# Optimization experiments

Measured on AMD Instinct MI355X. Metric: run time of the kernel, lower is better.

Reference implementation:

```python
import jax, jax.numpy as jnp
import numpy as np

B, NQ, NK, D = 16, 256, 256, 256  # batch, n_queries, n_keys, kq_size (=value_size)


def setup_inputs() -> dict:
    key = jax.random.key(0)
    ks = jax.random.split(key, 8)
    s1 = 1.0 / np.sqrt(2 * D)  # fan-in scaled init for W1 (split into Wk, Wq)
    s2 = 1.0 / np.sqrt(D)
    return {
        "keys": jax.random.normal(ks[0], (B, NK, D), jnp.float32),
        "queries": jax.random.normal(ks[1], (B, NQ, D), jnp.float32),
        "values": jax.random.normal(ks[2], (B, NK, D), jnp.float32),
        # MLP layer 1: Linear(2*D -> D); concat(keys, queries) @ W1 == keys@Wk + queries@Wq
        "Wk": jax.random.normal(ks[3], (D, D), jnp.float32) * s1,
        "Wq": jax.random.normal(ks[4], (D, D), jnp.float32) * s1,
        "b1": jax.random.normal(ks[5], (D,), jnp.float32) * 0.01,
        # MLP layer 2: Linear(D -> 1)
        "w2": jax.random.normal(ks[6], (D,), jnp.float32) * s2,
        "b2": jax.random.normal(ks[7], (1,), jnp.float32) * 0.01,
    }


def reference(keys, queries, values, Wk, Wq, b1, w2, b2):
    # Additive (Bahdanau) attention: score(q,k) = w2 . tanh(W1 @ [k; q] + b1) + b2
    hk = jnp.einsum("bkd,de->bke", keys, Wk)      # [B,K,D]
    hq = jnp.einsum("bqd,de->bqe", queries, Wq)   # [B,Q,D]
    h = jnp.tanh(hq[:, :, None, :] + hk[:, None, :, :] + b1)  # [B,Q,K,D]
    logits = jnp.einsum("bqkd,d->bqk", h, w2) + b2[0]          # [B,Q,K]
    attn = jax.nn.softmax(logits, axis=-1)                     # normalize over keys
    context = jnp.einsum("bqk,bkv->bqv", attn, values)         # [B,Q,Dv]
    return context
```

## Files before the change

### kernel.cpp

```cpp
#include <hip/hip_runtime.h>
#include <hip/hip_bf16.h>

#ifndef __has_builtin
#define __has_builtin(x) 0
#endif

__device__ __forceinline__ float fast_exp2(float x) {
#if __has_builtin(__builtin_amdgcn_exp2f)
  return __builtin_amdgcn_exp2f(x);
#else
  return __exp2f(x);
#endif
}
__device__ __forceinline__ float fast_rcp(float x) {
#if __has_builtin(__builtin_amdgcn_rcpf)
  return __builtin_amdgcn_rcpf(x);
#else
  return 1.0f / x;
#endif
}

#define B_   16
#define NQ_  256
#define NK_  256
#define D_   256
#define QT   4
#define TANH_SCALE 2.8853900817779268f
#define NEG2LOG2E  (-2.8853900817779268f)

__global__ __launch_bounds__(256) void proj_kernel(
    const float* __restrict__ queries, const float* __restrict__ keys,
    const float* __restrict__ Wq, const float* __restrict__ Wk,
    const float* __restrict__ b1,
    float* __restrict__ eqs, float* __restrict__ ekT)
{
  const int z = blockIdx.z;
  const float* __restrict__ X = z ? keys : queries;
  const float* __restrict__ W = z ? Wk : Wq;
  float* __restrict__ O = z ? ekT : eqs;

  const int m0 = blockIdx.x * 64;
  const int n0 = blockIdx.y * 64;
  const int t  = threadIdx.x;
  const int tx = t & 15, ty = t >> 4;

  __shared__ float As[64][68];
  __shared__ float Bs[64][68];

  float acc[4][4] = {};

  for (int kt = 0; kt < 4; ++kt) {
    const int k0 = kt * 64;
    #pragma unroll
    for (int i = 0; i < 4; ++i) {
      int f = t + 256 * i;
      int row = f >> 4;
      int kc  = (f & 15) << 2;
      *(float4*)&As[row][kc] = *(const float4*)&X[(size_t)(m0 + row) * D_ + (k0 + kc)];
    }
    #pragma unroll
    for (int i = 0; i < 4; ++i) {
      int f = t + 256 * i;
      int kr = f >> 4;
      int nc = (f & 15) << 2;
      *(float4*)&Bs[kr][nc] = *(const float4*)&W[(size_t)(k0 + kr) * D_ + (n0 + nc)];
    }
    __syncthreads();
    #pragma unroll 4
    for (int k4 = 0; k4 < 16; ++k4) {
      const int kk = k4 << 2;
      float4 a0 = *(const float4*)&As[(ty << 2) + 0][kk];
      float4 a1 = *(const float4*)&As[(ty << 2) + 1][kk];
      float4 a2 = *(const float4*)&As[(ty << 2) + 2][kk];
      float4 a3 = *(const float4*)&As[(ty << 2) + 3][kk];
      float4 b0 = *(const float4*)&Bs[kk + 0][tx << 2];
      float4 b1v = *(const float4*)&Bs[kk + 1][tx << 2];
      float4 b2 = *(const float4*)&Bs[kk + 2][tx << 2];
      float4 b3 = *(const float4*)&Bs[kk + 3][tx << 2];
      float A[4][4] = {{a0.x,a0.y,a0.z,a0.w},{a1.x,a1.y,a1.z,a1.w},
                       {a2.x,a2.y,a2.z,a2.w},{a3.x,a3.y,a3.z,a3.w}};
      float Bv[4][4] = {{b0.x,b0.y,b0.z,b0.w},{b1v.x,b1v.y,b1v.z,b1v.w},
                        {b2.x,b2.y,b2.z,b2.w},{b3.x,b3.y,b3.z,b3.w}};
      #pragma unroll
      for (int kkk = 0; kkk < 4; ++kkk)
        #pragma unroll
        for (int i = 0; i < 4; ++i)
          #pragma unroll
          for (int j = 0; j < 4; ++j)
            acc[i][j] = fmaf(A[i][kkk], Bv[kkk][j], acc[i][j]);
    }
    __syncthreads();
  }

  if (z == 0) {
    float bias[4];
    #pragma unroll
    for (int j = 0; j < 4; ++j) bias[j] = b1[n0 + (tx << 2) + j];
    #pragma unroll
    for (int i = 0; i < 4; ++i) {
      float4 o4;
      o4.x = fast_exp2(TANH_SCALE * (acc[i][0] + bias[0]));
      o4.y = fast_exp2(TANH_SCALE * (acc[i][1] + bias[1]));
      o4.z = fast_exp2(TANH_SCALE * (acc[i][2] + bias[2]));
      o4.w = fast_exp2(TANH_SCALE * (acc[i][3] + bias[3]));
      *(float4*)&O[(size_t)(m0 + (ty << 2) + i) * D_ + n0 + (tx << 2)] = o4;
    }
  } else {
    const int batch = m0 >> 8;
    const int key0  = (m0 & 255) + (ty << 2);
    #pragma unroll
    for (int j = 0; j < 4; ++j) {
      float4 o4;
      o4.x = fast_exp2(TANH_SCALE * acc[0][j]);
      o4.y = fast_exp2(TANH_SCALE * acc[1][j]);
      o4.z = fast_exp2(TANH_SCALE * acc[2][j]);
      o4.w = fast_exp2(TANH_SCALE * acc[3][j]);
      *(float4*)&O[((size_t)batch << 16) +
                   (size_t)(n0 + (tx << 2) + j) * NK_ + key0] = o4;
    }
  }
}

__global__ __launch_bounds__(256, 4) void attn_kernel(
    const float* __restrict__ eqs, const float* __restrict__ ekT,
    const float* __restrict__ values, const float* __restrict__ w2,
    float* __restrict__ out)
{
  const int wgid = blockIdx.x;
  const int b  = wgid & 15;
  const int q0 = (wgid >> 4) * QT;
  const int t  = threadIdx.x;
  const int lane = t & 63, wave = t >> 6;

  __shared__ float pvred[4][QT][D_];
  __shared__ float redB[4][QT];

  const float* __restrict__ ekTb  = ekT + ((size_t)b << 16);
  const float* __restrict__ equni = eqs + ((size_t)(b * NQ_) + q0) * D_;

  float acc[QT] = {};
  #pragma unroll 4
  for (int d4 = 0; d4 < D_ / 4; ++d4) {
    const int off = d4 << 2;
    float e0 = ekTb[(size_t)(off + 0) * NK_ + t];
    float e1 = ekTb[(size_t)(off + 1) * NK_ + t];
    float e2 = ekTb[(size_t)(off + 2) * NK_ + t];
    float e3 = ekTb[(size_t)(off + 3) * NK_ + t];
    float4 wv = *(const float4*)&w2[off];
    float w[4] = {wv.x, wv.y, wv.z, wv.w};
    #pragma unroll
    for (int qi = 0; qi < QT; ++qi) {
      float4 eqv = *(const float4*)&equni[(size_t)qi * D_ + off];
      float t0 = fmaf(eqv.x, e0, 1.0f);
      float t1 = fmaf(eqv.y, e1, 1.0f);
      float t2 = fmaf(eqv.z, e2, 1.0f);
      float t3 = fmaf(eqv.w, e3, 1.0f);
      float p01 = t0 * t1;
      float p23 = t2 * t3;
      float n01 = fmaf(w[1], t0, w[0] * t1);
      float n23 = fmaf(w[3], t2, w[2] * t3);
      float num = fmaf(n23, p01, n01 * p23);
      float r   = fast_rcp(p01 * p23);
      acc[qi] = fmaf(num, r, acc[qi]);
    }
  }

  float p[QT];
  #pragma unroll
  for (int qi = 0; qi < QT; ++qi)
    p[qi] = fast_exp2(NEG2LOG2E * acc[qi]);
  #pragma unroll
  for (int qi = 0; qi < QT; ++qi) {
    float v = p[qi];
    #pragma unroll
    for (int off = 32; off; off >>= 1) v += __shfl_xor(v, off, 64);
    if (lane == 0) redB[wave][qi] = v;
  }
  __syncthreads();
  float pl[QT];
  #pragma unroll
  for (int qi = 0; qi < QT; ++qi) {
    float inv = fast_rcp(redB[0][qi] + redB[1][qi] + redB[2][qi] + redB[3][qi]);
    pl[qi] = p[qi] * inv;
  }

  float ctx[QT][4] = {};
  const float* __restrict__ vbase =
      values + ((size_t)(b * NK_) + (wave << 6)) * D_ + (lane << 2);
  #pragma unroll 4
  for (int kl = 0; kl < 64; ++kl) {
    float4 vv = *(const float4*)&vbase[(size_t)kl * D_];
    float vz[4] = {vv.x, vv.y, vv.z, vv.w};
    #pragma unroll
    for (int qi = 0; qi < QT; ++qi) {
      float pk = __int_as_float(
          __builtin_amdgcn_readlane(__float_as_int(pl[qi]), kl));
      #pragma unroll
      for (int j = 0; j < 4; ++j)
        ctx[qi][j] = fmaf(pk, vz[j], ctx[qi][j]);
    }
  }

  #pragma unroll
  for (int qi = 0; qi < QT; ++qi)
    *(float4*)&pvred[wave][qi][lane << 2] =
        make_float4(ctx[qi][0], ctx[qi][1], ctx[qi][2], ctx[qi][3]);
  __syncthreads();
  #pragma unroll
  for (int qi = 0; qi < QT; ++qi) {
    float o = pvred[0][qi][t] + pvred[1][qi][t] +
              pvred[2][qi][t] + pvred[3][qi][t];
    out[((size_t)(b * NQ_) + q0 + qi) * D_ + t] = o;
  }
}

extern "C" void kernel_launch(void* const* d_in, const int* in_sizes, int n_in,
                              void* d_out, int out_size, void* d_ws, size_t ws_size,
                              hipStream_t stream)
{
  const float* keys    = (const float*)d_in[0];
  const float* queries = (const float*)d_in[1];
  const float* values  = (const float*)d_in[2];
  const float* Wk      = (const float*)d_in[3];
  const float* Wq      = (const float*)d_in[4];
  const float* b1      = (const float*)d_in[5];
  const float* w2      = (const float*)d_in[6];

  float* eqs = (float*)d_ws;
  float* ekT = eqs + (size_t)B_ * NQ_ * D_;
  float* out = (float*)d_out;

  dim3 pgrid(B_ * NQ_ / 64, D_ / 64, 2);
  proj_kernel<<<pgrid, 256, 0, stream>>>(queries, keys, Wq, Wk, b1, eqs, ekT);

  attn_kernel<<<dim3(B_ * NQ_ / QT), 256, 0, stream>>>(eqs, ekT, values, w2, out);
}
```

Baseline: 69.78 us.

## Split attention over key chunks into single-wave blocks with separate combine kernel

Replaces the 256-thread attention block with 4096 single-wave workgroups, each handling 4 queries against one 64-key chunk. Each workgroup writes partial context and partial softmax sums to workspace, and a new combine kernel adds the four chunks and normalises. This removes the LDS reductions and block barriers inside the attention kernel. In exchange it adds a third launch and a round trip of partial results through global memory. A fallback keeps the old single-block path, with a non-transposed key layout, when the workspace is too small.

New measurement: 69.75 us. About the same (-0.0%).

```diff
diff --git a/kernel.cpp b/kernel.cpp
--- a/kernel.cpp
+++ b/kernel.cpp
@@ -32,12 +32,12 @@
     const float* __restrict__ queries, const float* __restrict__ keys,
     const float* __restrict__ Wq, const float* __restrict__ Wk,
     const float* __restrict__ b1,
-    float* __restrict__ eqs, float* __restrict__ ekT)
+    float* __restrict__ eqs, float* __restrict__ ek_out, int tr)
 {
   const int z = blockIdx.z;
   const float* __restrict__ X = z ? keys : queries;
   const float* __restrict__ W = z ? Wk : Wq;
-  float* __restrict__ O = z ? ekT : eqs;
+  float* __restrict__ O = z ? ek_out : eqs;
 
   const int m0 = blockIdx.x * 64;
   const int n0 = blockIdx.y * 64;
@@ -105,7 +105,7 @@
       o4.w = fast_exp2(TANH_SCALE * (acc[i][3] + bias[3]));
       *(float4*)&O[(size_t)(m0 + (ty << 2) + i) * D_ + n0 + (tx << 2)] = o4;
     }
-  } else {
+  } else if (tr) {
     const int batch = m0 >> 8;
     const int key0  = (m0 & 255) + (ty << 2);
     #pragma unroll
@@ -118,22 +118,31 @@
       *(float4*)&O[((size_t)batch << 16) +
                    (size_t)(n0 + (tx << 2) + j) * NK_ + key0] = o4;
     }
-  }
-}
-
-__global__ __launch_bounds__(256, 4) void attn_kernel(
+  } else {
+    #pragma unroll
+    for (int i = 0; i < 4; ++i) {
+      float4 o4;
+      o4.x = fast_exp2(TANH_SCALE * acc[i][0]);
+      o4.y = fast_exp2(TANH_SCALE * acc[i][1]);
+      o4.z = fast_exp2(TANH_SCALE * acc[i][2]);
+      o4.w = fast_exp2(TANH_SCALE * acc[i][3]);
+      *(float4*)&O[(size_t)(m0 + (ty << 2) + i) * D_ + n0 + (tx << 2)] = o4;
+    }
+  }
+}
+
+__global__ __launch_bounds__(64) void attn_wave(
     const float* __restrict__ eqs, const float* __restrict__ ekT,
     const float* __restrict__ values, const float* __restrict__ w2,
-    float* __restrict__ out)
+    float* __restrict__ sctx, float* __restrict__ psum)
 {
   const int wgid = blockIdx.x;
-  const int b  = wgid & 15;
-  const int q0 = (wgid >> 4) * QT;
-  const int t  = threadIdx.x;
-  const int lane = t & 63, wave = t >> 6;
-
-  __shared__ float pvred[4][QT][D_];
-  __shared__ float redB[4][QT];
+  const int b    = wgid & 15;
+  const int qq   = (wgid >> 4) & 63;
+  const int kh   = wgid >> 10;
+  const int q0   = qq * QT;
+  const int k0   = kh * 64;
+  const int lane = threadIdx.x;
 
   const float* __restrict__ ekTb  = ekT + ((size_t)b << 16);
   const float* __restrict__ equni = eqs + ((size_t)(b * NQ_) + q0) * D_;
@@ -142,10 +151,11 @@
   #pragma unroll 4
   for (int d4 = 0; d4 < D_ / 4; ++d4) {
     const int off = d4 << 2;
-    float e0 = ekTb[(size_t)(off + 0) * NK_ + t];
-    float e1 = ekTb[(size_t)(off + 1) * NK_ + t];
-    float e2 = ekTb[(size_t)(off + 2) * NK_ + t];
-    float e3 = ekTb[(size_t)(off + 3) * NK_ + t];
+    const float* ekp = &ekTb[(size_t)off * NK_ + k0 + lane];
+    float e0 = ekp[0 * NK_];
+    float e1 = ekp[1 * NK_];
+    float e2 = ekp[2 * NK_];
+    float e3 = ekp[3 * NK_];
     float4 wv = *(const float4*)&w2[off];
     float w[4] = {wv.x, wv.y, wv.z, wv.w};
     #pragma unroll
@@ -160,8 +170,103 @@
       float n01 = fmaf(w[1], t0, w[0] * t1);
       float n23 = fmaf(w[3], t2, w[2] * t3);
       float num = fmaf(n23, p01, n01 * p23);
-      float r   = fast_rcp(p01 * p23);
-      acc[qi] = fmaf(num, r, acc[qi]);
+      acc[qi] = fmaf(num, fast_rcp(p01 * p23), acc[qi]);
+    }
+  }
+
+  float p[QT], s[QT];
+  #pragma unroll
+  for (int qi = 0; qi < QT; ++qi) {
+    p[qi] = fast_exp2(NEG2LOG2E * acc[qi]);
+    float v = p[qi];
+    #pragma unroll
+    for (int off = 32; off; off >>= 1) v += __shfl_xor(v, off, 64);
+    s[qi] = v;
+  }
+  if (lane == 0)
+    *(float4*)&psum[(size_t)wgid * 4] = make_float4(s[0], s[1], s[2], s[3]);
+
+  float ctx[QT][4] = {};
+  const float* __restrict__ vbase =
+      values + ((size_t)(b * NK_) + k0) * D_ + (lane << 2);
+  #pragma unroll 4
+  for (int i = 0; i < 64; ++i) {
+    float4 vv = *(const float4*)&vbase[(size_t)i * D_];
+    float vz[4] = {vv.x, vv.y, vv.z, vv.w};
+    #pragma unroll
+    for (int qi = 0; qi < QT; ++qi) {
+      float pk = __int_as_float(
+          __builtin_amdgcn_readlane(__float_as_int(p[qi]), i));
+      #pragma unroll
+      for (int j = 0; j < 4; ++j)
+        ctx[qi][j] = fmaf(pk, vz[j], ctx[qi][j]);
+    }
+  }
+  #pragma unroll
+  for (int qi = 0; qi < QT; ++qi)
+    *(float4*)&sctx[((size_t)wgid * 4 + qi) * D_ + (lane << 2)] =
+        make_float4(ctx[qi][0], ctx[qi][1], ctx[qi][2], ctx[qi][3]);
+}
+
+__global__ __launch_bounds__(256) void combine_kernel(
+    const float* __restrict__ sctx, const float* __restrict__ psum,
+    float* __restrict__ out)
+{
+  const int bid = blockIdx.x;
+  const int b = bid & 15, qq = bid >> 4;
+  const int t = threadIdx.x;
+
+  #pragma unroll
+  for (int qi = 0; qi < QT; ++qi) {
+    float s = 0.f, o = 0.f;
+    #pragma unroll
+    for (int kh = 0; kh < 4; ++kh) {
+      const size_t wg = (size_t)(kh * 1024 + bid);
+      s += psum[wg * 4 + qi];
+      o += sctx[(wg * 4 + qi) * D_ + t];
+    }
+    out[((size_t)(b * NQ_) + qq * QT + qi) * D_ + t] = o * fast_rcp(s);
+  }
+}
+
+__global__ __launch_bounds__(256, 4) void attn_fallback(
+    const float* __restrict__ eqs, const float* __restrict__ eks,
+    const float* __restrict__ values, const float* __restrict__ w2,
+    float* __restrict__ out)
+{
+  const int wgid = blockIdx.x;
+  const int b  = wgid & 15;
+  const int q0 = (wgid >> 4) * QT;
+  const int t  = threadIdx.x;
+  const int lane = t & 63, wave = t >> 6;
+
+  __shared__ float pvred[4][QT][D_];
+  __shared__ float redB[4][QT];
+
+  const float* __restrict__ ekrow = eks + ((size_t)(b * NK_) + t) * D_;
+  const float* __restrict__ equni = eqs + ((size_t)(b * NQ_) + q0) * D_;
+
+  float acc[QT] = {};
+  #pragma unroll 4
+  for (int d4 = 0; d4 < D_ / 4; ++d4) {
+    const int off = d4 << 2;
+    float4 ekv = *(const float4*)&ekrow[off];
+    float4 wv  = *(const float4*)&w2[off];
+    float e[4] = {ekv.x, ekv.y, ekv.z, ekv.w};
+    float w[4] = {wv.x, wv.y, wv.z, wv.w};
+    #pragma unroll
+    for (int qi = 0; qi < QT; ++qi) {
+      float4 eqv = *(const float4*)&equni[(size_t)qi * D_ + off];
+      float t0 = fmaf(eqv.x, e[0], 1.0f);
+      float t1 = fmaf(eqv.y, e[1], 1.0f);
+      float t2 = fmaf(eqv.z, e[2], 1.0f);
+      float t3 = fmaf(eqv.w, e[3], 1.0f);
+      float p01 = t0 * t1;
+      float p23 = t2 * t3;
+      float n01 = fmaf(w[1], t0, w[0] * t1);
+      float n23 = fmaf(w[3], t2, w[2] * t3);
+      float num = fmaf(n23, p01, n01 * p23);
+      acc[qi] = fmaf(num, fast_rcp(p01 * p23), acc[qi]);
     }
   }
 
@@ -226,12 +331,24 @@
   const float* b1      = (const float*)d_in[5];
   const float* w2      = (const float*)d_in[6];
 
-  float* eqs = (float*)d_ws;
-  float* ekT = eqs + (size_t)B_ * NQ_ * D_;
-  float* out = (float*)d_out;
+  float* eqs  = (float*)d_ws;
+  float* ekb  = eqs + (size_t)B_ * NQ_ * D_;
+  float* sctx = ekb + (size_t)B_ * NK_ * D_;
+  float* psum = sctx + (size_t)4096 * 4 * 256;
+  float* out  = (float*)d_out;
+
+  const size_t need = ((size_t)2 * B_ * NQ_ * D_ + (size_t)4096 * 4 * 256 +
+                       (size_t)4096 * 4) * sizeof(float);
+  const int use_wave = (ws_size >= need) ? 1 : 0;
 
   dim3 pgrid(B_ * NQ_ / 64, D_ / 64, 2);
-  proj_kernel<<<pgrid, 256, 0, stream>>>(queries, keys, Wq, Wk, b1, eqs, ekT);
-
-  attn_kernel<<<dim3(B_ * NQ_ / QT), 256, 0, stream>>>(eqs, ekT, values, w2, out);
-}
+  proj_kernel<<<pgrid, 256, 0, stream>>>(queries, keys, Wq, Wk, b1,
+                                         eqs, ekb, use_wave);
+
+  if (use_wave) {
+    attn_wave<<<dim3(4096), 64, 0, stream>>>(eqs, ekb, values, w2, sctx, psum);
+    combine_kernel<<<dim3(1024), 256, 0, stream>>>(sctx, psum, out);
+  } else {
+    attn_fallback<<<dim3(B_ * NQ_ / QT), 256, 0, stream>>>(eqs, ekb, values, w2, out);
+  }
+}
```
